# Optimization experiments

Hardware: AMD Instinct MI355X
Metric: run time of the kernel (lower is better)

## Reference

```python
import jax, jax.numpy as jnp
import numpy as np

B, CIN, COUT, T, H, W = 2, 16, 16, 31, 128, 128


def setup_inputs() -> dict:
    key = jax.random.key(0)
    k1, k2 = jax.random.split(key)
    x = jax.random.normal(k1, (B, CIN, T, H, W), dtype=jnp.float32)
    conv_w = jax.random.normal(k2, (6 * COUT, CIN, 3, 3, 3), dtype=jnp.float32) * 0.05
    conv_b = jnp.zeros((6 * COUT,), dtype=jnp.float32)
    return {"x": x, "conv_w": conv_w, "conv_b": conv_b}


def _sru_scan(f, r, wx, xs):
    """Elementwise SRU recurrence along leading (time) axis.
    All args [T, B, C, H, W].  C_0 = 1 - f_0 (per original code);
    C_t = f_t*C_{t-1} + (1-f_t)*wx_t ;  h_t = r_t*C_t + (1-r_t)*x_t.
    """
    C0 = 1.0 - f[0]
    h0 = r[0] * C0 + (1.0 - r[0]) * xs[0]

    def step(C, inp):
        ft, rt, wxt, xt = inp
        C = ft * C + (1.0 - ft) * wxt
        h = rt * C + (1.0 - rt) * xt
        return C, h

    _, hs = jax.lax.scan(step, C0, (f[1:], r[1:], wx[1:], xs[1:]))
    return jnp.concatenate([h0[None], hs], axis=0)  # [T,B,C,H,W]


def reference(x, conv_w, conv_b):
    # Conv3d: NCDHW, k=3, s=1, p=1 -> shape-preserving, 6*COUT output channels
    gates = jax.lax.conv_general_dilated(
        x, conv_w, window_strides=(1, 1, 1), padding=[(1, 1)] * 3,
        dimension_numbers=("NCDHW", "OIDHW", "NCDHW"))
    gates = gates + conv_b[None, :, None, None, None]

    Wx, ft, ft2, rt, rt2, X = jnp.split(gates, 6, axis=1)
    Wx = jnp.tanh(Wx)
    ft = jax.nn.sigmoid(ft)
    ft2 = jax.nn.sigmoid(ft2)
    rt = jax.nn.sigmoid(rt)
    rt2 = jax.nn.sigmoid(rt2)
    X = jnp.tanh(X)  # act == 'tanh'

    # move band axis (dim 2) to the front for scanning: [T,B,C,H,W]
    tfirst = lambda a: jnp.moveaxis(a, 2, 0)
    Wx_t, ft_t, ft2_t, rt_t, rt2_t, X_t = map(tfirst, (Wx, ft, ft2, rt, rt2, X))

    # left-to-right pass (ft, rt)
    htl = _sru_scan(ft_t, rt_t, Wx_t, X_t)
    # right-to-left pass (ft2, rt2): scan on reversed sequences, reverse back
    rev = lambda a: a[::-1]
    htr = rev(_sru_scan(rev(ft2_t), rev(rt2_t), rev(Wx_t), rev(X_t)))

    out = htl + htr  # [T,B,C,H,W]
    return jnp.moveaxis(out, 0, 2)  # [B,C,T,H,W]
```

## Files before the change

### kernel.cpp

```cpp
#include <hip/hip_runtime.h>

#define DEVFN __device__ __forceinline__

typedef __attribute__((ext_vector_type(8))) short short8;
typedef __attribute__((ext_vector_type(4))) float floatx4;
typedef unsigned short u16;
typedef unsigned int u32;

typedef __attribute__((address_space(1))) const void gas_void;
typedef __attribute__((address_space(3))) void las_void;

constexpr int B_   = 2;
constexpr int CIN  = 16;
constexpr int COUT = 16;
constexpr int T_   = 31;
constexpr int H_   = 128;
constexpr int W_   = 128;
constexpr int OC   = 6 * COUT;
constexpr int HW   = H_ * W_;
constexpr int KVOL = CIN * 27;
constexpr int KP   = 448;

constexpr int TP = T_ + 2;
constexpr int HP = H_ + 2;
constexpr int WP = W_ + 2;
constexpr int Sh = WP * 16;
constexpr int St = HP * Sh;
constexpr int NPAD  = B_ * TP * HP * WP;
constexpr int NPADX = NPAD + HP * WP;
constexpr int PADBLK = (NPADX + 255) / 256;
constexpr int WBLK   = (OC * KP + 255) / 256;

constexpr int APH = 7 * 6 * 4 * 16 * 8;

constexpr int XCHUNK = 34 * 3 * 20;
constexpr int XT_OFF = APH;
constexpr int XT_U16 = 2048 * 8;
constexpr int LDS_U16 = APH + XT_U16;

constexpr int GSTR = 268;
constexpr int GS   = 16 * GSTR;
constexpr int GLDS = 6 * GS;

DEVFN float sigmoid_(float v) { return 1.f / (1.f + __expf(-v)); }
DEVFN float tanh_(float v)    { return 1.f - 2.f / (__expf(2.f * v) + 1.f); }

DEVFN u16 f2h(float v) {
  _Float16 h = (_Float16)v;
  u16 u; __builtin_memcpy(&u, &h, 2); return u;
}
DEVFN float h2f(u16 u) {
  _Float16 h; __builtin_memcpy(&h, &u, 2); return (float)h;
}

__global__ __launch_bounds__(256) void prep_kernel(const float* __restrict__ x,
                                                   const float* __restrict__ cw,
                                                   u16* __restrict__ xh,
                                                   u16* __restrict__ wr) {
  if (blockIdx.x < PADBLK) {
    const int idx = blockIdx.x * 256 + threadIdx.x;
    if (idx >= NPADX) return;
    int r = idx;
    const int ww = r % WP; r /= WP;
    const int hh = r % HP; r /= HP;
    const int tt = r % TP; const int b = r / TP;
    const bool in_ = (b < B_) & (tt >= 1) & (tt <= T_) & (hh >= 1) &
                     (hh <= H_) & (ww >= 1) & (ww <= W_);
    const int ts = in_ ? tt - 1 : 0, hs = in_ ? hh - 1 : 0,
              ws = in_ ? ww - 1 : 0;
    const int bs = in_ ? b : 0;
    const float* xp = x + ((size_t)bs * CIN * T_ + ts) * HW + hs * W_ + ws;
    u32 ph[8];
#pragma unroll
    for (int ci = 0; ci < 16; ++ci) {
      const float v = in_ ? xp[ci * (T_ * HW)] : 0.f;
      const u16 hu = f2h(v);
      if (ci & 1) ph[ci >> 1] |= ((u32)hu) << 16;
      else        ph[ci >> 1] = hu;
    }
    uint4* dh = (uint4*)(xh + (size_t)idx * 16);
    dh[0] = make_uint4(ph[0], ph[1], ph[2], ph[3]);
    dh[1] = make_uint4(ph[4], ph[5], ph[6], ph[7]);
  } else {
    const int idx = (blockIdx.x - PADBLK) * 256 + threadIdx.x;
    if (idx >= OC * KP) return;
    const int j    = idx & 7;
    const int n    = (idx >> 3) & 15;
    const int quad = (idx >> 7) & 3;
    const int m    = (idx >> 9) % 6;
    const int s    = idx / 3072;
    const int oc   = m * 16 + n;
    const int k    = s * 32 + quad * 8 + j;
    const int off  = k >> 4, ci = k & 15;
    const float v  = (off < 27) ? cw[oc * KVOL + ci * 27 + off] : 0.f;
    wr[idx] = f2h(v);
  }
}

template <int PH>
DEVFN void kphase(const u16* __restrict__ As, const u16* __restrict__ xt,
                  const int (&bb)[4], int n, int quad, int qhalf,
                  floatx4 (&acc)[6][4]) {
#pragma unroll
  for (int sl = 0; sl < 7; ++sl) {
    const int s  = PH * 7 + sl;
    const int oE = 2 * s;
    const int oO = (2 * s + 1 < 27) ? (2 * s + 1) : 26;
    const int dE = (oE / 9) * 960 + ((oE % 9) / 3) * 320 + (oE % 3) * 32;
    const int dO = (oO / 9) * 960 + ((oO % 9) / 3) * 320 + (oO % 3) * 32;
    const int d  = qhalf ? dO : dE;
    short8 bh[4];
#pragma unroll
    for (int j = 0; j < 4; ++j)
      bh[j] = *(const short8*)((const char*)xt + (bb[j] + d));
#pragma unroll
    for (int m = 0; m < 6; ++m) {
      const short8 a =
          *(const short8*)(As + (sl * 6 + m) * 512 + quad * 128 + n * 8);
#pragma unroll
      for (int j = 0; j < 4; ++j)
        acc[m][j] =
            __builtin_amdgcn_mfma_f32_16x16x32_f16(a, bh[j], acc[m][j], 0, 0, 0);
    }
  }
}

__global__ __launch_bounds__(256, 2) void conv_sru_fused(
    const u16* __restrict__ xh, const u16* __restrict__ wr,
    const float* __restrict__ cb, float* __restrict__ out) {
  const int lane = threadIdx.x & 63, wv = threadIdx.x >> 6;
  const int n = lane & 15, quad = lane >> 4;
  const int qhalf = quad >> 1, cihalf = quad & 1;
  const int th = n >> 3, wloc = n & 7;
  const int wbase = blockIdx.x * 8;
  const int h = blockIdx.y;
  const int b = blockIdx.z;

  __shared__ __align__(16) u16 Ls[LDS_U16];
  u16* As = Ls;
  u16* xt = Ls + XT_OFF;

  {
    const u16* xgb = xh + ((size_t)(b * TP) * HP + h) * WP * 16 +
                     (size_t)wbase * 16;
#pragma unroll
    for (int it = 0; it < 8; ++it) {
      const int cl = it * 256 + (int)threadIdx.x;
      const int c = (cl < XCHUNK) ? cl : (XCHUNK - 1);
      const int strip = c / 20;
      const int o16 = c - strip * 20;
      const int tt = strip / 3;
      const int hh = strip - tt * 3;
      const u16* src = xgb + (size_t)tt * St + hh * Sh + o16 * 8;
      __builtin_amdgcn_global_load_lds((gas_void*)src,
                                       (las_void*)(xt + (size_t)cl * 8), 16, 0,
                                       0);
    }
  }

  int bb[4];
#pragma unroll
  for (int j = 0; j < 4; ++j)
    bb[j] = (wv * 8 + j * 2 + th) * 960 + wloc * 32 + cihalf * 16;

  floatx4 acc[6][4];
#pragma unroll
  for (int m = 0; m < 6; ++m)
#pragma unroll
    for (int j = 0; j < 4; ++j) acc[m][j] = (floatx4)(0.f);

  for (int i = threadIdx.x; i < APH / 8; i += 256)
    ((uint4*)As)[i] = ((const uint4*)wr)[i];
  __syncthreads();
  kphase<0>(As, xt, bb, n, quad, qhalf, acc);

  __syncthreads();
  for (int i = threadIdx.x; i < APH / 8; i += 256)
    ((uint4*)As)[i] = ((const uint4*)(wr + APH))[i];
  __syncthreads();
  kphase<1>(As, xt, bb, n, quad, qhalf, acc);

  __syncthreads();
#pragma unroll
  for (int m = 0; m < 6; ++m) {
    const bool isTanh = (m == 0) || (m == 5);
#pragma unroll
    for (int rr = 0; rr < 4; ++rr) {
      const int c = quad * 4 + rr;
      const float bias = cb[m * 16 + c];
#pragma unroll
      for (int j = 0; j < 4; ++j) {
        const int t = wv * 8 + j * 2 + th;
        float v = acc[m][j][rr] + bias;
        v = isTanh ? tanh_(v) : sigmoid_(v);
        Ls[(m * 16 + c) * GSTR + t * 8 + wloc] = f2h(v);
      }
    }
  }
  __syncthreads();

  const int tid  = threadIdx.x;
  const int half = tid >> 7;
  const int ser  = tid & 127;
  const int c = ser >> 3, w = ser & 7;
  const int gb = c * GSTR + w;

  if (half == 0) {
    float C = 0.f;
#pragma unroll
    for (int t = 0; t < T_; ++t) {
      const float wx = h2f(Ls[0 * GS + gb + t * 8]);
      const float f  = h2f(Ls[1 * GS + gb + t * 8]);
      const float r  = h2f(Ls[3 * GS + gb + t * 8]);
      const float xv = h2f(Ls[5 * GS + gb + t * 8]);
      C = (t == 0) ? (1.f - f) : (f * C + (1.f - f) * wx);
      const float htl = r * C + (1.f - r) * xv;
      const u32 bits = __float_as_uint(htl);
      Ls[1 * GS + gb + t * 8] = (u16)(bits & 0xffffu);
      Ls[3 * GS + gb + t * 8] = (u16)(bits >> 16);
    }
  } else {
    float C2 = 0.f;
#pragma unroll
    for (int t = T_ - 1; t >= 0; --t) {
      const float wx = h2f(Ls[0 * GS + gb + t * 8]);
      const float f2 = h2f(Ls[2 * GS + gb + t * 8]);
      const float r2 = h2f(Ls[4 * GS + gb + t * 8]);
      const float xv = h2f(Ls[5 * GS + gb + t * 8]);
      C2 = (t == T_ - 1) ? (1.f - f2) : (f2 * C2 + (1.f - f2) * wx);
      const float htr = r2 * C2 + (1.f - r2) * xv;
      const u32 bits = __float_as_uint(htr);
      Ls[2 * GS + gb + t * 8] = (u16)(bits & 0xffffu);
      Ls[4 * GS + gb + t * 8] = (u16)(bits >> 16);
    }
  }
  __syncthreads();

  {
    const int tlo = half ? 16 : 0;
    const int thi = half ? T_ : 16;
    const size_t ob = ((size_t)(b * COUT + c) * T_) * HW + h * W_ + wbase + w;
    for (int t = tlo; t < thi; ++t) {
      const u32 l1 = Ls[1 * GS + gb + t * 8];
      const u32 h1 = Ls[3 * GS + gb + t * 8];
      const u32 l2 = Ls[2 * GS + gb + t * 8];
      const u32 h2 = Ls[4 * GS + gb + t * 8];
      out[ob + (size_t)t * HW] =
          __uint_as_float(l1 | (h1 << 16)) + __uint_as_float(l2 | (h2 << 16));
    }
  }
}

__global__ __launch_bounds__(256) void sru_scan_kernel(
    const u16* __restrict__ g, float* __restrict__ out) {
  const int idx  = blockIdx.x * 256 + threadIdx.x;
  const int sp   = idx & (HW - 1);
  const int bc   = idx >> 14;
  const int base = bc * (T_ * HW) + sp;
  const int P    = B_ * COUT * T_ * HW;

  const u16* gWx = g + 0 * P + base;
  const u16* gF  = g + 1 * P + base;
  const u16* gF2 = g + 2 * P + base;
  const u16* gR  = g + 3 * P + base;
  const u16* gR2 = g + 4 * P + base;
  const u16* gX  = g + 5 * P + base;

  float wxs[T_], xs[T_], htl[T_];
  float C = 0.f;
#pragma unroll
  for (int t = 0; t < T_; ++t) {
    const float wx = h2f(gWx[t * HW]);
    const float f  = h2f(gF[t * HW]);
    const float r  = h2f(gR[t * HW]);
    const float xv = h2f(gX[t * HW]);
    wxs[t] = wx;
    xs[t]  = xv;
    C = (t == 0) ? (1.f - f) : (f * C + (1.f - f) * wx);
    htl[t] = r * C + (1.f - r) * xv;
  }
  float C2 = 0.f;
#pragma unroll
  for (int t = T_ - 1; t >= 0; --t) {
    const float f2 = h2f(gF2[t * HW]);
    const float r2 = h2f(gR2[t * HW]);
    C2 = (t == T_ - 1) ? (1.f - f2) : (f2 * C2 + (1.f - f2) * wxs[t]);
    const float htr = r2 * C2 + (1.f - r2) * xs[t];
    out[base + t * HW] = htl[t] + htr;
  }
}

__global__ __launch_bounds__(256) void conv_gates_kernel(
    const float* __restrict__ x, const float* __restrict__ cw,
    const float* __restrict__ cb, u16* __restrict__ gates) {
  const int sp = blockIdx.x * 256 + threadIdx.x;
  const int oc = blockIdx.y;
  const int bt = blockIdx.z;
  const int b  = bt / T_;
  const int t  = bt - b * T_;
  const int h  = sp >> 7;
  const int wc = sp & (W_ - 1);

  __shared__ float wsh[KVOL];
  for (int i = threadIdx.x; i < KVOL; i += 256) wsh[i] = cw[oc * KVOL + i];
  __syncthreads();

  float acc = cb[oc];
  const float* xb = x + b * (CIN * T_ * HW);
  for (int ci = 0; ci < CIN; ++ci) {
    const float* xc = xb + ci * (T_ * HW);
#pragma unroll
    for (int kd = 0; kd < 3; ++kd) {
      const int tt = t + kd - 1;
      if ((unsigned)tt >= (unsigned)T_) continue;
      const float* xt = xc + tt * HW;
#pragma unroll
      for (int kh = 0; kh < 3; ++kh) {
        const int hh = h + kh - 1;
        if ((unsigned)hh >= (unsigned)H_) continue;
        const float* xr = xt + hh * W_;
        const float* wrp = &wsh[(ci * 3 + kd) * 9 + kh * 3];
        if (wc > 0)      acc += wrp[0] * xr[wc - 1];
        acc += wrp[1] * xr[wc];
        if (wc < W_ - 1) acc += wrp[2] * xr[wc + 1];
      }
    }
  }
  const int g = oc >> 4, c = oc & 15;
  const float av = (g == 0 || g == 5) ? tanh_(acc) : sigmoid_(acc);
  const int off = (((g * B_ + b) * COUT + c) * T_ + t) * HW + sp;
  gates[off] = f2h(av);
}

extern "C" void kernel_launch(void* const* d_in, const int* in_sizes, int n_in,
                              void* d_out, int out_size, void* d_ws,
                              size_t ws_size, hipStream_t stream) {
  (void)in_sizes; (void)n_in; (void)out_size;
  const float* x  = (const float*)d_in[0];
  const float* cw = (const float*)d_in[1];
  const float* cb = (const float*)d_in[2];
  float* out = (float*)d_out;

  const size_t planeElems = (size_t)B_ * COUT * T_ * HW;
  const size_t szGatesH = 6 * planeElems * sizeof(u16);
  const size_t szX      = (size_t)NPADX * 16 * sizeof(u16);
  const size_t szW      = (size_t)OC * KP * sizeof(u16);

  char* p = (char*)d_ws;
  if (ws_size >= szX + szW) {
    u16* xh  = (u16*)p;
    u16* wrp = (u16*)(p + szX);
    prep_kernel<<<PADBLK + WBLK, 256, 0, stream>>>(x, cw, xh, wrp);
    const dim3 gfused(W_ / 8, H_, B_);
    conv_sru_fused<<<gfused, 256, 0, stream>>>(xh, wrp, cb, out);
  } else if (ws_size >= szGatesH) {
    u16* gates = (u16*)p;
    const dim3 gdir(HW / 256, OC, B_ * T_);
    conv_gates_kernel<<<gdir, 256, 0, stream>>>(x, cw, cb, gates);
    const int scanBlocks = (B_ * COUT * HW) / 256;
    sru_scan_kernel<<<scanBlocks, 256, 0, stream>>>(gates, out);
  }
}
```

Baseline: 276.6 us.

## Read conv input directly from global with register prefetch pipeline instead of LDS staging

The x halo tile is no longer staged into LDS. Each lane now reads its B-operand fragments straight from global memory (padded fp16 layout) into rotating register buffers, prefetching two k-slices ahead of the MFMAs. Weight chunks are copied into LDS with global_load_lds rather than through registers. This removes the x staging and its LDS footprint, which may allow more occupancy, but the global loads are scattered and rely on the cache for the reuse that LDS used to provide. It also keeps more registers live for the prefetch buffers.

```diff
diff --git a/kernel.cpp b/kernel.cpp
--- a/kernel.cpp
+++ b/kernel.cpp
@@ -32,11 +32,7 @@
 constexpr int WBLK   = (OC * KP + 255) / 256;
 
 constexpr int APH = 7 * 6 * 4 * 16 * 8;
-
-constexpr int XCHUNK = 34 * 3 * 20;
-constexpr int XT_OFF = APH;
-constexpr int XT_U16 = 2048 * 8;
-constexpr int LDS_U16 = APH + XT_U16;
+constexpr int ACHUNK = APH / 8;
 
 constexpr int GSTR = 268;
 constexpr int GS   = 16 * GSTR;
@@ -51,6 +47,11 @@
 }
 DEVFN float h2f(u16 u) {
   _Float16 h; __builtin_memcpy(&h, &u, 2); return (float)h;
+}
+
+DEVFN constexpr int dOff(int off) {
+  const int o = (off < 27) ? off : 26;
+  return (o / 9) * St + ((o % 9) / 3) * Sh + (o % 3) * 16;
 }
 
 __global__ __launch_bounds__(256) void prep_kernel(const float* __restrict__ x,
@@ -97,33 +98,25 @@
   }
 }
 
-template <int PH>
-DEVFN void kphase(const u16* __restrict__ As, const u16* __restrict__ xt,
-                  const int (&bb)[4], int n, int quad, int qhalf,
-                  floatx4 (&acc)[6][4]) {
-#pragma unroll
-  for (int sl = 0; sl < 7; ++sl) {
-    const int s  = PH * 7 + sl;
-    const int oE = 2 * s;
-    const int oO = (2 * s + 1 < 27) ? (2 * s + 1) : 26;
-    const int dE = (oE / 9) * 960 + ((oE % 9) / 3) * 320 + (oE % 3) * 32;
-    const int dO = (oO / 9) * 960 + ((oO % 9) / 3) * 320 + (oO % 3) * 32;
-    const int d  = qhalf ? dO : dE;
-    short8 bh[4];
-#pragma unroll
-    for (int j = 0; j < 4; ++j)
-      bh[j] = *(const short8*)((const char*)xt + (bb[j] + d));
-#pragma unroll
-    for (int m = 0; m < 6; ++m) {
-      const short8 a =
-          *(const short8*)(As + (sl * 6 + m) * 512 + quad * 128 + n * 8);
-#pragma unroll
-      for (int j = 0; j < 4; ++j)
-        acc[m][j] =
-            __builtin_amdgcn_mfma_f32_16x16x32_f16(a, bh[j], acc[m][j], 0, 0, 0);
-    }
-  }
-}
+#define LOADB(s, q)                                                       \
+  do {                                                                    \
+    const int d_ = qhalf ? dOff(2 * (s) + 1) : dOff(2 * (s));             \
+    q[0] = *(const short8*)(xp0 + d_);                                    \
+    q[1] = *(const short8*)(xp1 + d_);                                    \
+    q[2] = *(const short8*)(xp2 + d_);                                    \
+    q[3] = *(const short8*)(xp3 + d_);                                    \
+  } while (0)
+
+#define MFMAS(sl, q)                                                      \
+  do {                                                                    \
+    _Pragma("unroll") for (int m_ = 0; m_ < 6; ++m_) {                    \
+      const short8 a_ =                                                   \
+          *(const short8*)(As + ((sl)*6 + m_) * 512 + quad * 128 + n * 8);\
+      _Pragma("unroll") for (int j_ = 0; j_ < 4; ++j_)                    \
+          acc[m_][j_] = __builtin_amdgcn_mfma_f32_16x16x32_f16(           \
+              a_, q[j_], acc[m_][j_], 0, 0, 0);                           \
+    }                                                                     \
+  } while (0)
 
 __global__ __launch_bounds__(256, 2) void conv_sru_fused(
     const u16* __restrict__ xh, const u16* __restrict__ wr,
@@ -136,49 +129,67 @@
   const int h = blockIdx.y;
   const int b = blockIdx.z;
 
-  __shared__ __align__(16) u16 Ls[LDS_U16];
+  __shared__ __align__(16) u16 Ls[GLDS];
   u16* As = Ls;
-  u16* xt = Ls + XT_OFF;
-
+
+  const u16 *xp0, *xp1, *xp2, *xp3;
   {
-    const u16* xgb = xh + ((size_t)(b * TP) * HP + h) * WP * 16 +
-                     (size_t)wbase * 16;
-#pragma unroll
-    for (int it = 0; it < 8; ++it) {
-      const int cl = it * 256 + (int)threadIdx.x;
-      const int c = (cl < XCHUNK) ? cl : (XCHUNK - 1);
-      const int strip = c / 20;
-      const int o16 = c - strip * 20;
-      const int tt = strip / 3;
-      const int hh = strip - tt * 3;
-      const u16* src = xgb + (size_t)tt * St + hh * Sh + o16 * 8;
-      __builtin_amdgcn_global_load_lds((gas_void*)src,
-                                       (las_void*)(xt + (size_t)cl * 8), 16, 0,
+    const int t0 = wv * 8 + th;
+    const size_t pb =
+        ((size_t)((b * TP + t0) * HP + h) * WP + wbase + wloc) * 16 +
+        cihalf * 8;
+    xp0 = xh + pb;
+    xp1 = xh + pb + (size_t)2 * St;
+    xp2 = xh + pb + (size_t)4 * St;
+    xp3 = xh + pb + (size_t)6 * St;
+  }
+
+  floatx4 acc[6][4];
+#pragma unroll
+  for (int m = 0; m < 6; ++m)
+#pragma unroll
+    for (int j = 0; j < 4; ++j) acc[m][j] = (floatx4)(0.f);
+
+#pragma unroll
+  for (int it = 0; it < 11; ++it) {
+    const int i = it * 256 + (int)threadIdx.x;
+    if (i < ACHUNK)
+      __builtin_amdgcn_global_load_lds((gas_void*)(wr + (size_t)i * 8),
+                                       (las_void*)(As + (size_t)i * 8), 16, 0,
                                        0);
-    }
-  }
-
-  int bb[4];
-#pragma unroll
-  for (int j = 0; j < 4; ++j)
-    bb[j] = (wv * 8 + j * 2 + th) * 960 + wloc * 32 + cihalf * 16;
-
-  floatx4 acc[6][4];
-#pragma unroll
-  for (int m = 0; m < 6; ++m)
-#pragma unroll
-    for (int j = 0; j < 4; ++j) acc[m][j] = (floatx4)(0.f);
-
-  for (int i = threadIdx.x; i < APH / 8; i += 256)
-    ((uint4*)As)[i] = ((const uint4*)wr)[i];
-  __syncthreads();
-  kphase<0>(As, xt, bb, n, quad, qhalf, acc);
-
-  __syncthreads();
-  for (int i = threadIdx.x; i < APH / 8; i += 256)
-    ((uint4*)As)[i] = ((const uint4*)(wr + APH))[i];
-  __syncthreads();
-  kphase<1>(As, xt, bb, n, quad, qhalf, acc);
+  }
+
+  short8 bq0[4], bq1[4], bq2[4];
+  LOADB(0, bq0);
+  LOADB(1, bq1);
+  __syncthreads();
+
+  LOADB(2, bq2);  MFMAS(0, bq0);
+  LOADB(3, bq0);  MFMAS(1, bq1);
+  LOADB(4, bq1);  MFMAS(2, bq2);
+  LOADB(5, bq2);  MFMAS(3, bq0);
+  LOADB(6, bq0);  MFMAS(4, bq1);
+  LOADB(7, bq1);  MFMAS(5, bq2);
+  LOADB(8, bq2);  MFMAS(6, bq0);
+
+  __syncthreads();
+#pragma unroll
+  for (int it = 0; it < 11; ++it) {
+    const int i = it * 256 + (int)threadIdx.x;
+    if (i < ACHUNK)
+      __builtin_amdgcn_global_load_lds((gas_void*)(wr + APH + (size_t)i * 8),
+                                       (las_void*)(As + (size_t)i * 8), 16, 0,
+                                       0);
+  }
+  __syncthreads();
+
+  LOADB(9, bq0);   MFMAS(0, bq1);
+  LOADB(10, bq1);  MFMAS(1, bq2);
+  LOADB(11, bq2);  MFMAS(2, bq0);
+  LOADB(12, bq0);  MFMAS(3, bq1);
+  LOADB(13, bq1);  MFMAS(4, bq2);
+                   MFMAS(5, bq0);
+                   MFMAS(6, bq1);
 
   __syncthreads();
 #pragma unroll
```

Result: faster. 259.1 us (-6.3%).
